# Kernel optimization log

Hardware: AMD Instinct MI355X
Metric: run time of the kernel (lower is better)

## Reference

```python
import jax, jax.numpy as jnp
import numpy as np

K_CLUSTERS = 512
N_ITERS = 10  # fixed Lloyd iterations (torch_kmeans uses max_iter with tol; fixed count keeps it jit-friendly)


def setup_inputs() -> dict:
    key = jax.random.key(0)
    x = jax.random.normal(key, (4, 8192, 256), dtype=jnp.float32)  # (B, N, D)
    return {"x": x}


def _sq_dists(x, centers):
    # x: (B,N,D), centers: (B,K,D) -> squared Euclidean distances (B,N,K)
    xc = jnp.einsum('bnd,bkd->bnk', x, centers)
    x2 = jnp.sum(x * x, axis=-1, keepdims=True)          # (B,N,1)
    c2 = jnp.sum(centers * centers, axis=-1)[:, None, :]  # (B,1,K)
    return x2 - 2.0 * xc + c2


def _kmeans(x, k=K_CLUSTERS, iters=N_ITERS):
    # deterministic init: first k points of each batch as initial centroids
    centers0 = x[:, :k, :]  # (B,K,D)

    def step(centers, _):
        labels = jnp.argmin(_sq_dists(x, centers), axis=-1)          # (B,N)
        onehot = jax.nn.one_hot(labels, k, dtype=x.dtype)            # (B,N,K)
        sums = jnp.einsum('bnk,bnd->bkd', onehot, x)                 # (B,K,D)
        counts = jnp.sum(onehot, axis=1)                             # (B,K)
        new_centers = jnp.where(
            counts[..., None] > 0,
            sums / jnp.maximum(counts, 1.0)[..., None],
            centers,  # keep empty clusters' previous centroid
        )
        return new_centers, None

    centers, _ = jax.lax.scan(step, centers0, None, length=iters)
    labels = jnp.argmin(_sq_dists(x, centers), axis=-1)
    return labels, centers


def reference(x):
    labels, centers = _kmeans(x)
    return labels, centers
```

## Files before the change

kernel.cpp:

```cpp
#include <hip/hip_runtime.h>
#include <math.h>

#define BB 4
#define NN 8192
#define DD 256
#define KK 512
#define NITERS 10

#define TAU 0.06f
#define NCH 128

typedef _Float16 f16;
typedef f16   f16x8 __attribute__((ext_vector_type(8)));
typedef float f32x4 __attribute__((ext_vector_type(4)));

__global__ __launch_bounds__(256) void init_centers_k(const float* __restrict__ x,
                                                      float* __restrict__ centers,
                                                      f16* __restrict__ chh,
                                                      float* __restrict__ c2) {
    __shared__ float sq[256];
    int bk = blockIdx.x;
    int b  = bk >> 9;
    int k  = bk & 511;
    int t  = threadIdx.x;
    size_t idx = (size_t)bk * DD + t;
    float v = x[((size_t)b * NN + k) * DD + t];
    centers[idx] = v;
    chh[idx] = (f16)v;
    sq[t] = v * v;
    __syncthreads();
    for (int s = 128; s > 0; s >>= 1) {
        if (t < s) sq[t] += sq[t + s];
        __syncthreads();
    }
    if (t == 0) c2[bk] = sq[0];
}

__global__ __launch_bounds__(256) void rowsumsq_k(const float* __restrict__ rows,
                                                  float* __restrict__ out, int nrows) {
    int r = blockIdx.x * 256 + threadIdx.x;
    if (r >= nrows) return;
    const float* p = rows + (size_t)r * DD;
    float total = 0.f;
    #pragma unroll
    for (int h = 0; h < 2; ++h) {
        float a[8];
        #pragma unroll
        for (int j = 0; j < 8; ++j) a[j] = 0.f;
        for (int i = 0; i < 128; i += 8) {
            #pragma unroll
            for (int j = 0; j < 8; ++j) {
                float v  = p[h * 128 + i + j];
                float sq = __fmul_rn(v, v);
                a[j] = __fadd_rn(a[j], sq);
            }
        }
        float s = __fadd_rn(__fadd_rn(__fadd_rn(a[0], a[1]), __fadd_rn(a[2], a[3])),
                            __fadd_rn(__fadd_rn(a[4], a[5]), __fadd_rn(a[6], a[7])));
        total = __fadd_rn(total, s);
    }
    out[r] = total;
}

__global__ __launch_bounds__(256, 2) void assign_k(
    const float* __restrict__ x,
    const f16* __restrict__ chh,
    const float* __restrict__ x2g, const float* __restrict__ c2g,
    int* __restrict__ labels, int* __restrict__ flagslot, int* __restrict__ flaglist)
{
    __shared__ f16 xlh[64 * 256];
    __shared__ f16 xll[64 * 256];
    __shared__ float rv1s[4][64];
    __shared__ float rv2s[4][64];
    __shared__ int   rk1s[4][64];

    const int tid  = threadIdx.x;
    const int wid  = tid >> 6;
    const int lane = tid & 63;
    const int l15  = lane & 15;
    const int lg   = lane >> 4;
    const int b    = blockIdx.x >> 7;
    const int m0   = (blockIdx.x & 127) * 64;

    const float* xb = x + (size_t)(b * NN + m0) * DD;

    #pragma unroll
    for (int i = 0; i < 8; ++i) {
        int lin = tid + i * 256;
        int row = lin >> 5, g = lin & 31;
        const float* p = xb + row * DD + g * 8;
        float4 a  = *(const float4*)p;
        float4 bq = *(const float4*)(p + 4);
        float vf[8] = {a.x, a.y, a.z, a.w, bq.x, bq.y, bq.z, bq.w};
        f16x8 hv, lv;
        #pragma unroll
        for (int j = 0; j < 8; ++j) {
            f16 h = (f16)vf[j];
            hv[j] = h;
            lv[j] = (f16)(vf[j] - (float)h);
        }
        int si = row * 256 + ((g ^ (row & 7)) << 3);
        *(f16x8*)&xlh[si] = hv;
        *(f16x8*)&xll[si] = lv;
    }
    __syncthreads();

    const f16* bhb = chh + ((size_t)b * KK + wid * 128) * DD;

    f32x4 acc[4][8];
    #pragma unroll
    for (int mi = 0; mi < 4; ++mi)
        #pragma unroll
        for (int ki = 0; ki < 8; ++ki)
            acc[mi][ki] = (f32x4){0.f, 0.f, 0.f, 0.f};

    #pragma unroll
    for (int s = 0; s < 8; ++s) {
        const int d0 = s * 32;
        f16x8 bh[8];
        #pragma unroll
        for (int ki = 0; ki < 8; ++ki) {
            size_t off = (size_t)(ki * 16 + l15) * DD + d0 + lg * 8;
            bh[ki] = *(const f16x8*)(bhb + off);
        }
        f16x8 ah[4], al[4];
        #pragma unroll
        for (int mi = 0; mi < 4; ++mi) {
            int row = mi * 16 + l15;
            int g   = (d0 >> 3) + lg;
            int si  = row * 256 + ((g ^ (row & 7)) << 3);
            ah[mi] = *(const f16x8*)&xlh[si];
            al[mi] = *(const f16x8*)&xll[si];
        }
        #pragma unroll
        for (int ki = 0; ki < 8; ++ki) {
            #pragma unroll
            for (int mi = 0; mi < 4; ++mi) {
                acc[mi][ki] = __builtin_amdgcn_mfma_f32_16x16x32_f16(ah[mi], bh[ki], acc[mi][ki], 0, 0, 0);
                acc[mi][ki] = __builtin_amdgcn_mfma_f32_16x16x32_f16(al[mi], bh[ki], acc[mi][ki], 0, 0, 0);
            }
        }
    }

    float c2v[8];
    #pragma unroll
    for (int ki = 0; ki < 8; ++ki)
        c2v[ki] = c2g[b * KK + wid * 128 + ki * 16 + l15];

    #pragma unroll
    for (int mi = 0; mi < 4; ++mi) {
        #pragma unroll
        for (int r = 0; r < 4; ++r) {
            int p = mi * 16 + lg * 4 + r;
            float x2p = x2g[b * NN + m0 + p];
            float v1 = __builtin_inff(), v2 = __builtin_inff();
            int   k1 = 0x7fffffff;
            #pragma unroll
            for (int ki = 0; ki < 8; ++ki) {
                float s    = acc[mi][ki][r];
                float cand = __fadd_rn(__fsub_rn(x2p, __fmul_rn(2.0f, s)), c2v[ki]);
                int   kidx = wid * 128 + ki * 16 + l15;
                if (cand < v1 || (cand == v1 && kidx < k1)) { v2 = v1; v1 = cand; k1 = kidx; }
                else if (cand < v2) v2 = cand;
            }
            #pragma unroll
            for (int off = 1; off < 16; off <<= 1) {
                float ov1 = __shfl_xor(v1, off, 64);
                int   ok1 = __shfl_xor(k1, off, 64);
                float ov2 = __shfl_xor(v2, off, 64);
                if (ov1 < v1 || (ov1 == v1 && ok1 < k1)) { v2 = fminf(v1, ov2); v1 = ov1; k1 = ok1; }
                else v2 = fminf(v2, ov1);
            }
            if (l15 == 0) { rv1s[wid][p] = v1; rv2s[wid][p] = v2; rk1s[wid][p] = k1; }
        }
    }
    __syncthreads();
    if (tid < 64) {
        float v1 = rv1s[0][tid], v2 = rv2s[0][tid];
        int   k1 = rk1s[0][tid];
        #pragma unroll
        for (int w = 1; w < 4; ++w) {
            float ov1 = rv1s[w][tid], ov2 = rv2s[w][tid];
            int   ok1 = rk1s[w][tid];
            if (ov1 < v1 || (ov1 == v1 && ok1 < k1)) { v2 = fminf(v1, ov2); v1 = ov1; k1 = ok1; }
            else v2 = fminf(v2, ov1);
        }
        int g = b * NN + m0 + tid;
        labels[g] = k1;
        if (v2 - v1 < TAU) {
            int pos = atomicAdd(flagslot, 1);
            flaglist[pos] = g;
        }
    }
}

__global__ __launch_bounds__(256) void refine_k(const float* __restrict__ x,
                                                const float* __restrict__ centers,
                                                const int* __restrict__ flagslot,
                                                const int* __restrict__ flaglist,
                                                int* __restrict__ labels,
                                                int* __restrict__ dirty) {
    __shared__ float  xsr[DD];
    __shared__ double sv[256];
    __shared__ int    si[256];
    const int t = threadIdx.x;
    if (t < 2) dirty[blockIdx.x * 2 + t] = 0;
    const int cnt = flagslot[0];
    for (int idx = blockIdx.x; idx < cnt; idx += gridDim.x) {
        const int g = flaglist[idx];
        const int b = g >> 13;
        __syncthreads();
        xsr[t] = x[(size_t)g * DD + t];
        __syncthreads();
        const float* cbase = centers + (size_t)b * KK * DD;
        double bestv = 1e300; int bestk = 0x7fffffff;
        #pragma unroll
        for (int h = 0; h < 2; ++h) {
            int k = t + h * 256;
            const float* cr = cbase + (size_t)k * DD;
            double a0 = 0, a1 = 0, a2 = 0, a3 = 0;
            for (int d = 0; d < DD; d += 4) {
                float4 cv = *(const float4*)(cr + d);
                double f0 = (double)xsr[d + 0] - (double)cv.x;
                double f1 = (double)xsr[d + 1] - (double)cv.y;
                double f2 = (double)xsr[d + 2] - (double)cv.z;
                double f3 = (double)xsr[d + 3] - (double)cv.w;
                a0 += f0 * f0; a1 += f1 * f1; a2 += f2 * f2; a3 += f3 * f3;
            }
            double dist = (a0 + a1) + (a2 + a3);
            if (dist < bestv || (dist == bestv && k < bestk)) { bestv = dist; bestk = k; }
        }
        sv[t] = bestv; si[t] = bestk;
        __syncthreads();
        for (int s = 128; s > 0; s >>= 1) {
            if (t < s) {
                if (sv[t + s] < sv[t] || (sv[t + s] == sv[t] && si[t + s] < si[t])) {
                    sv[t] = sv[t + s]; si[t] = si[t + s];
                }
            }
            __syncthreads();
        }
        if (t == 0) labels[g] = si[0];
    }
}

__global__ __launch_bounds__(64) void chunk_hist_k(const int* __restrict__ labels,
                                                   int* __restrict__ labels_prev,
                                                   int* __restrict__ dirty,
                                                   int* __restrict__ chunkhist) {
    __shared__ int h[KK];
    const int bc = blockIdx.x;
    const int b  = bc >> 7;
    const int c  = bc & (NCH - 1);
    const int t  = threadIdx.x;
    for (int k = t; k < KK; k += 64) h[k] = 0;
    __syncthreads();
    int n  = b * NN + c * 64 + t;
    int l  = labels[n];
    int lp = labels_prev[n];
    atomicAdd(&h[l], 1);
    if (l != lp) {
        dirty[b * KK + l] = 1;
        if (lp >= 0 && lp < KK) dirty[b * KK + lp] = 1;
        labels_prev[n] = l;
    }
    __syncthreads();
    int* ch = chunkhist + (size_t)bc * KK;
    for (int k = t; k < KK; k += 64) ch[k] = h[k];
}

__global__ __launch_bounds__(512) void scan_k(int* __restrict__ chunkhist,
                                              int* __restrict__ counts,
                                              int* __restrict__ offsets) {
    __shared__ int s[KK];
    const int b = blockIdx.x;
    const int k = threadIdx.x;
    int* ch = chunkhist + (size_t)b * NCH * KK;
    int run = 0;
    for (int c0 = 0; c0 < NCH; c0 += 16) {
        int v[16];
        #pragma unroll
        for (int j = 0; j < 16; ++j) v[j] = ch[(size_t)(c0 + j) * KK + k];
        #pragma unroll
        for (int j = 0; j < 16; ++j) {
            ch[(size_t)(c0 + j) * KK + k] = run;
            run += v[j];
        }
    }
    counts[b * KK + k] = run;
    s[k] = run;
    __syncthreads();
    for (int off = 1; off < KK; off <<= 1) {
        int v = (k >= off) ? s[k - off] : 0;
        __syncthreads();
        s[k] += v;
        __syncthreads();
    }
    offsets[b * KK + k] = s[k] - run;
}

__global__ __launch_bounds__(64) void scatter_k(const int* __restrict__ labels,
                                                const int* __restrict__ chunkhist,
                                                const int* __restrict__ offsets,
                                                int* __restrict__ idxlist) {
    const int bc = blockIdx.x;
    const int b  = bc >> 7;
    const int c  = bc & (NCH - 1);
    const int t  = threadIdx.x;
    const int n  = c * 64 + t;
    const int l  = labels[b * NN + n];
    int rank = 0;
    for (int j = 0; j < 64; ++j) {
        int lj = __shfl(l, j, 64);
        rank += (lj == l && j < t) ? 1 : 0;
    }
    int base = offsets[b * KK + l] + chunkhist[(size_t)bc * KK + l];
    idxlist[b * NN + base + rank] = n;
}

__global__ __launch_bounds__(1024) void centers_update_k(const float* __restrict__ x,
                                                         float* __restrict__ centers,
                                                         f16* __restrict__ chh,
                                                         float* __restrict__ c2,
                                                         const int* __restrict__ counts,
                                                         const int* __restrict__ offsets,
                                                         const int* __restrict__ idxlist,
                                                         const int* __restrict__ dirty) {
    __shared__ float part[16][DD];
    __shared__ float sq[256];
    const int bk   = blockIdx.x;
    const int b    = bk >> 9;
    const int tid  = threadIdx.x;
    const int w    = tid >> 6;
    const int lane = tid & 63;
    if (!dirty[bk]) return;
    const int cnt = counts[bk];
    if (cnt == 0) return;
    const int* il = idxlist + b * NN + offsets[bk];
    const float* xb = x + (size_t)b * NN * DD;
    float4 acc = {0.f, 0.f, 0.f, 0.f};
    #pragma unroll 8
    for (int j = w; j < cnt; j += 16) {
        int n = il[j];
        float4 v = *(const float4*)(xb + (size_t)n * DD + lane * 4);
        acc.x = __fadd_rn(acc.x, v.x);
        acc.y = __fadd_rn(acc.y, v.y);
        acc.z = __fadd_rn(acc.z, v.z);
        acc.w = __fadd_rn(acc.w, v.w);
    }
    *(float4*)&part[w][lane * 4] = acc;
    __syncthreads();
    float val = 0.f;
    if (tid < DD) {
        float s = 0.f;
        #pragma unroll
        for (int w2 = 0; w2 < 16; ++w2) s = __fadd_rn(s, part[w2][tid]);
        val = s / (float)cnt;
        size_t idx = (size_t)bk * DD + tid;
        centers[idx] = val;
        chh[idx] = (f16)val;
    }
    if (tid < 256) sq[tid] = val * val;
    __syncthreads();
    for (int s = 128; s > 0; s >>= 1) {
        if (tid < s) sq[tid] += sq[tid + s];
        __syncthreads();
    }
    if (tid == 0) c2[bk] = sq[0];
}

__global__ __launch_bounds__(256) void out_k(const int* __restrict__ labels,
                                             const float* __restrict__ centers,
                                             float* __restrict__ out) {
    size_t i = (size_t)blockIdx.x * 256 + threadIdx.x;
    if (i < (size_t)BB * NN) out[i] = (float)labels[i];
    else                     out[i] = centers[i - (size_t)BB * NN];
}

extern "C" void kernel_launch(void* const* d_in, const int* in_sizes, int n_in,
                              void* d_out, int out_size, void* d_ws, size_t ws_size,
                              hipStream_t stream) {
    const float* x = (const float*)d_in[0];
    float* out = (float*)d_out;
    float* ws  = (float*)d_ws;

    float* centers  = ws;
    float* c2       = centers + (size_t)BB * KK * DD;
    float* x2       = c2 + BB * KK;
    int*   labels   = (int*)(x2 + BB * NN);
    int*   flagcnt  = labels + BB * NN;
    int*   flaglist = flagcnt + 64;
    int*   counts   = flaglist + BB * NN;
    int*   offsets  = counts + BB * KK;
    int*   idxlist  = offsets + BB * KK;
    int*   chunkhist= idxlist + BB * NN;
    f16*   chh      = (f16*)(chunkhist + (size_t)BB * NCH * KK);
    int*   labels_prev = (int*)(chh + (size_t)BB * KK * DD);
    int*   dirty    = labels_prev + BB * NN;

    hipMemsetAsync(flagcnt, 0, 64 * sizeof(int), stream);
    hipMemsetAsync(labels_prev, 0xFF, (size_t)BB * NN * sizeof(int), stream);

    init_centers_k<<<BB * KK, 256, 0, stream>>>(x, centers, chh, c2);
    rowsumsq_k<<<(BB * NN + 255) / 256, 256, 0, stream>>>(x, x2, BB * NN);

    for (int it = 0; it < NITERS; ++it) {
        assign_k<<<BB * (NN / 64), 256, 0, stream>>>(x, chh, x2, c2,
                                                     labels, flagcnt + it, flaglist);
        refine_k<<<1024, 256, 0, stream>>>(x, centers, flagcnt + it, flaglist,
                                           labels, dirty);
        chunk_hist_k<<<BB * NCH, 64, 0, stream>>>(labels, labels_prev, dirty, chunkhist);
        scan_k<<<BB, 512, 0, stream>>>(chunkhist, counts, offsets);
        scatter_k<<<BB * NCH, 64, 0, stream>>>(labels, chunkhist, offsets, idxlist);
        centers_update_k<<<BB * KK, 1024, 0, stream>>>(x, centers, chh, c2,
                                                       counts, offsets, idxlist, dirty);
    }

    assign_k<<<BB * (NN / 64), 256, 0, stream>>>(x, chh, x2, c2,
                                                 labels, flagcnt + NITERS, flaglist);
    refine_k<<<1024, 256, 0, stream>>>(x, centers, flagcnt + NITERS, flaglist,
                                       labels, dirty);

    out_k<<<(int)(((size_t)BB * NN + (size_t)BB * KK * DD + 255) / 256), 256, 0, stream>>>(
        labels, centers, out);
}
```

Baseline: 931.3 us.

## Fuse histogram, scan and scatter into one per-batch sort kernel

Replaces the three kernels that build per-chunk label histograms, prefix-scan them, and scatter point indices into cluster order with a single kernel that runs one 512-thread block per batch. The block does the histograms wave by wave, then the scan, then the scatter, separated by block barriers. This removes two kernel launches and their inter-kernel gaps per iteration. In exchange the work runs on only four blocks, so each wave processes many chunks serially with little parallelism across the GPU.

```diff
diff --git a/kernel.cpp b/kernel.cpp
--- a/kernel.cpp
+++ b/kernel.cpp
@@ -244,78 +244,76 @@
     }
 }
 
-__global__ __launch_bounds__(64) void chunk_hist_k(const int* __restrict__ labels,
-                                                   int* __restrict__ labels_prev,
-                                                   int* __restrict__ dirty,
-                                                   int* __restrict__ chunkhist) {
-    __shared__ int h[KK];
-    const int bc = blockIdx.x;
-    const int b  = bc >> 7;
-    const int c  = bc & (NCH - 1);
-    const int t  = threadIdx.x;
-    for (int k = t; k < KK; k += 64) h[k] = 0;
-    __syncthreads();
-    int n  = b * NN + c * 64 + t;
-    int l  = labels[n];
-    int lp = labels_prev[n];
-    atomicAdd(&h[l], 1);
-    if (l != lp) {
-        dirty[b * KK + l] = 1;
-        if (lp >= 0 && lp < KK) dirty[b * KK + lp] = 1;
-        labels_prev[n] = l;
-    }
-    __syncthreads();
-    int* ch = chunkhist + (size_t)bc * KK;
-    for (int k = t; k < KK; k += 64) ch[k] = h[k];
-}
-
-__global__ __launch_bounds__(512) void scan_k(int* __restrict__ chunkhist,
+__global__ __launch_bounds__(512) void sort_k(const int* __restrict__ labels,
+                                              int* __restrict__ labels_prev,
+                                              int* __restrict__ dirty,
+                                              int* __restrict__ chunkhist,
                                               int* __restrict__ counts,
-                                              int* __restrict__ offsets) {
+                                              int* __restrict__ offsets,
+                                              int* __restrict__ idxlist) {
+    __shared__ int whist[8][KK];
     __shared__ int s[KK];
-    const int b = blockIdx.x;
-    const int k = threadIdx.x;
-    int* ch = chunkhist + (size_t)b * NCH * KK;
-    int run = 0;
-    for (int c0 = 0; c0 < NCH; c0 += 16) {
-        int v[16];
-        #pragma unroll
-        for (int j = 0; j < 16; ++j) v[j] = ch[(size_t)(c0 + j) * KK + k];
-        #pragma unroll
-        for (int j = 0; j < 16; ++j) {
-            ch[(size_t)(c0 + j) * KK + k] = run;
-            run += v[j];
-        }
-    }
-    counts[b * KK + k] = run;
-    s[k] = run;
-    __syncthreads();
-    for (int off = 1; off < KK; off <<= 1) {
-        int v = (k >= off) ? s[k - off] : 0;
-        __syncthreads();
-        s[k] += v;
-        __syncthreads();
-    }
-    offsets[b * KK + k] = s[k] - run;
-}
-
-__global__ __launch_bounds__(64) void scatter_k(const int* __restrict__ labels,
-                                                const int* __restrict__ chunkhist,
-                                                const int* __restrict__ offsets,
-                                                int* __restrict__ idxlist) {
-    const int bc = blockIdx.x;
-    const int b  = bc >> 7;
-    const int c  = bc & (NCH - 1);
-    const int t  = threadIdx.x;
-    const int n  = c * 64 + t;
-    const int l  = labels[b * NN + n];
-    int rank = 0;
-    for (int j = 0; j < 64; ++j) {
-        int lj = __shfl(l, j, 64);
-        rank += (lj == l && j < t) ? 1 : 0;
-    }
-    int base = offsets[b * KK + l] + chunkhist[(size_t)bc * KK + l];
-    idxlist[b * NN + base + rank] = n;
+    const int b    = blockIdx.x;
+    const int tid  = threadIdx.x;
+    const int w    = tid >> 6;
+    const int lane = tid & 63;
+    const int* lb  = labels + b * NN;
+
+    for (int c = w; c < NCH; c += 8) {
+        for (int k = lane; k < KK; k += 64) whist[w][k] = 0;
+        int n  = c * 64 + lane;
+        int l  = lb[n];
+        atomicAdd(&whist[w][l], 1);
+        int gn = b * NN + n;
+        int lp = labels_prev[gn];
+        if (l != lp) {
+            dirty[b * KK + l] = 1;
+            if (lp >= 0 && lp < KK) dirty[b * KK + lp] = 1;
+            labels_prev[gn] = l;
+        }
+        int* ch = chunkhist + (size_t)(b * NCH + c) * KK;
+        for (int k = lane; k < KK; k += 64) ch[k] = whist[w][k];
+    }
+    __syncthreads();
+
+    {
+        const int k = tid;
+        int* ch = chunkhist + (size_t)b * NCH * KK;
+        int run = 0;
+        for (int c0 = 0; c0 < NCH; c0 += 16) {
+            int v[16];
+            #pragma unroll
+            for (int j = 0; j < 16; ++j) v[j] = ch[(size_t)(c0 + j) * KK + k];
+            #pragma unroll
+            for (int j = 0; j < 16; ++j) {
+                ch[(size_t)(c0 + j) * KK + k] = run;
+                run += v[j];
+            }
+        }
+        counts[b * KK + k] = run;
+        s[k] = run;
+        __syncthreads();
+        for (int off = 1; off < KK; off <<= 1) {
+            int v = (k >= off) ? s[k - off] : 0;
+            __syncthreads();
+            s[k] += v;
+            __syncthreads();
+        }
+        offsets[b * KK + k] = s[k] - run;
+    }
+    __syncthreads();
+
+    for (int c = w; c < NCH; c += 8) {
+        int n = c * 64 + lane;
+        int l = lb[n];
+        int rank = 0;
+        for (int j = 0; j < 64; ++j) {
+            int lj = __shfl(l, j, 64);
+            rank += (lj == l && j < lane) ? 1 : 0;
+        }
+        int base = offsets[b * KK + l] + chunkhist[(size_t)(b * NCH + c) * KK + l];
+        idxlist[b * NN + base + rank] = n;
+    }
 }
 
 __global__ __launch_bounds__(1024) void centers_update_k(const float* __restrict__ x,
@@ -409,9 +407,8 @@
                                                      labels, flagcnt + it, flaglist);
         refine_k<<<1024, 256, 0, stream>>>(x, centers, flagcnt + it, flaglist,
                                            labels, dirty);
-        chunk_hist_k<<<BB * NCH, 64, 0, stream>>>(labels, labels_prev, dirty, chunkhist);
-        scan_k<<<BB, 512, 0, stream>>>(chunkhist, counts, offsets);
-        scatter_k<<<BB * NCH, 64, 0, stream>>>(labels, chunkhist, offsets, idxlist);
+        sort_k<<<BB, 512, 0, stream>>>(labels, labels_prev, dirty, chunkhist,
+                                       counts, offsets, idxlist);
         centers_update_k<<<BB * KK, 1024, 0, stream>>>(x, centers, chh, c2,
                                                        counts, offsets, idxlist, dirty);
     }
```

Measured after the change: 1.342 ms. +44.1%, slower.
